# Kernel tuning notes

Hardware: AMD Instinct MI355X
Metric: run time of the kernel (lower is better)

Reference implementation:

```python
import jax, jax.numpy as jnp
import numpy as np

WINDOW_SIZE = 5
CONSISTENCY_WEIGHT = 1.0


def _wsum(x, w):
    # sliding-window sum along axis 1 via exclusive cumsum differences
    s = jnp.cumsum(x, axis=1)
    s = jnp.pad(s, ((0, 0), (1, 0)))
    return s[:, w:] - s[:, :-w]  # [B, L-w+1]


def setup_inputs() -> dict:
    key = jax.random.key(0)
    k1, k2, k3 = jax.random.split(key, 3)
    B, L, C = 512, 16384, 2
    return {
        "predictions": jax.random.normal(k1, (B, L, C), dtype=jnp.float32),
        "targets": jax.random.randint(k2, (B, L), 0, 2, dtype=jnp.int32),
        "mask": jax.random.randint(k3, (B, L), 0, 2, dtype=jnp.int32),
    }


def reference(predictions, targets, mask):
    w = WINDOW_SIZE
    probs = jax.nn.softmax(predictions, axis=-1)[..., 1]  # [B, L]
    t = targets.astype(jnp.float32)
    m = mask.astype(jnp.float32)

    msum = _wsum(m, w)                       # [B, W]
    denom = jnp.maximum(msum, 1.0)           # clamp(min=1.0)
    spm = _wsum(probs * m, w)
    stm = _wsum(t * m, w)
    sp2m = _wsum(probs * probs * m, w)
    st2m = _wsum(t * t * m, w)

    pmean = spm / denom
    tmean = stm / denom
    # masked biased variance: sum((x - mean)^2 * m) / clamp(msum, 1)
    pvar = (sp2m - 2.0 * pmean * spm + pmean * pmean * msum) / denom
    tvar = (st2m - 2.0 * tmean * stm + tmean * tmean * msum) / denom

    mse = jnp.mean((pvar - tvar) ** 2, axis=0)          # per-window MSE over batch, [W]
    valid = (jnp.sum(msum, axis=0) > 0).astype(jnp.float32)  # skip windows with zero mask
    cnt = jnp.maximum(jnp.sum(valid), 1.0)
    loss = jnp.sum(mse * valid) / cnt * CONSISTENCY_WEIGHT
    return loss
```

## Files before the change

kernel.cpp:

```cpp
#include <hip/hip_runtime.h>
#include <math.h>

#define BATCH 512
#define LEN   16384
#define WIN   5
#define WOUT  (LEN - WIN + 1)
#define TPB   128
#define WPT   4
#define WPB   (TPB * WPT)
#define EPT   (WPT + WIN - 1)

__global__ __launch_bounds__(TPB)
void bcl_partial_kernel(const float* __restrict__ pred,
                        const int*   __restrict__ tgt,
                        const int*   __restrict__ msk,
                        float* __restrict__ part_d2,
                        float* __restrict__ part_ms,
                        int bper) {
    const int j0 = blockIdx.x * WPB + (int)threadIdx.x * WPT;
    if (j0 >= WOUT) return;
    const int b0 = blockIdx.y * bper;

    float accd2[WPT] = {0.f, 0.f, 0.f, 0.f};
    float accms[WPT] = {0.f, 0.f, 0.f, 0.f};

    for (int b = b0; b < b0 + bper; ++b) {
        const size_t base = (size_t)b * LEN + j0;

        const int4 m0 = *(const int4*)(msk + base);
        const int4 m1 = *(const int4*)(msk + base + 4);
        const int4 t0 = *(const int4*)(tgt + base);
        const int4 t1 = *(const int4*)(tgt + base + 4);
        const float4 q0 = *(const float4*)(pred + base * 2);
        const float4 q1 = *(const float4*)(pred + base * 2 + 4);
        const float4 q2 = *(const float4*)(pred + base * 2 + 8);
        const float4 q3 = *(const float4*)(pred + base * 2 + 12);

        float m[EPT], tm[EPT], pm[EPT], p2m[EPT];
        {
            const int mi[EPT] = {m0.x, m0.y, m0.z, m0.w, m1.x, m1.y, m1.z, m1.w};
            const int ti[EPT] = {t0.x, t0.y, t0.z, t0.w, t1.x, t1.y, t1.z, t1.w};
            const float dx[EPT] = {q0.x - q0.y, q0.z - q0.w,
                                   q1.x - q1.y, q1.z - q1.w,
                                   q2.x - q2.y, q2.z - q2.w,
                                   q3.x - q3.y, q3.z - q3.w};
#pragma unroll
            for (int i = 0; i < EPT; ++i) {
                const float p  = 1.0f / (1.0f + __expf(dx[i]));
                const float mf = (float)mi[i];
                m[i]   = mf;
                tm[i]  = (float)(ti[i] & mi[i]);
                pm[i]  = p * mf;
                p2m[i] = p * p * mf;
            }
        }

#pragma unroll
        for (int w = 0; w < WPT; ++w) {
            float msum = 0.f, stm = 0.f, spm = 0.f, sp2m = 0.f;
#pragma unroll
            for (int k = 0; k < WIN; ++k) {
                msum += m[w + k];
                stm  += tm[w + k];
                spm  += pm[w + k];
                sp2m += p2m[w + k];
            }
            const float denom = fmaxf(msum, 1.0f);
            const float inv   = 1.0f / denom;
            const float pmean = spm * inv;
            const float tmean = stm * inv;
            const float pvar  = (sp2m - 2.0f * pmean * spm + pmean * pmean * msum) * inv;
            const float tvar  = (stm  - 2.0f * tmean * stm + tmean * tmean * msum) * inv;
            const float d = pvar - tvar;
            accd2[w] += d * d;
            accms[w] += msum;
        }
    }

    *(float4*)(part_d2 + (size_t)blockIdx.y * WOUT + j0) =
        make_float4(accd2[0], accd2[1], accd2[2], accd2[3]);
    *(float4*)(part_ms + (size_t)blockIdx.y * WOUT + j0) =
        make_float4(accms[0], accms[1], accms[2], accms[3]);
}

__global__ void bcl_window_reduce(const float* __restrict__ part_d2,
                                  const float* __restrict__ part_ms,
                                  double* __restrict__ accum,
                                  unsigned int* __restrict__ ticket,
                                  float* __restrict__ out,
                                  int nchunks) {
    const int j = blockIdx.x * blockDim.x + threadIdx.x;
    double num = 0.0, cnt = 0.0;
    if (j < WOUT) {
        float d2 = 0.f, ms = 0.f;
        for (int c = 0; c < nchunks; ++c) {
            d2 += part_d2[(size_t)c * WOUT + j];
            ms += part_ms[(size_t)c * WOUT + j];
        }
        if (ms > 0.f) {
            num = (double)d2 * (1.0 / (double)BATCH);
            cnt = 1.0;
        }
    }
    for (int off = 32; off > 0; off >>= 1) {
        num += __shfl_down(num, off, 64);
        cnt += __shfl_down(cnt, off, 64);
    }
    __shared__ double s_num[4], s_cnt[4];
    const int lane = threadIdx.x & 63, wave = threadIdx.x >> 6;
    if (lane == 0) { s_num[wave] = num; s_cnt[wave] = cnt; }
    __syncthreads();
    if (threadIdx.x == 0) {
        double n = 0.0, c = 0.0;
        const int nw = (int)(blockDim.x >> 6);
        for (int wv = 0; wv < nw; ++wv) { n += s_num[wv]; c += s_cnt[wv]; }
        atomicAdd(&accum[0], n);
        atomicAdd(&accum[1], c);
        __threadfence();
        const unsigned int t = atomicAdd(ticket, 1u);
        if (t == gridDim.x - 1) {
            out[0] = (float)(accum[0] / fmax(accum[1], 1.0));
        }
    }
}

extern "C" void kernel_launch(void* const* d_in, const int* in_sizes, int n_in,
                              void* d_out, int out_size, void* d_ws, size_t ws_size,
                              hipStream_t stream) {
    const float* pred = (const float*)d_in[0];
    const int*   tgt  = (const int*)d_in[1];
    const int*   msk  = (const int*)d_in[2];
    float* out = (float*)d_out;

    int nchunks = 64;
    while (nchunks > 1) {
        size_t need = (size_t)nchunks * WOUT * 2 * sizeof(float) + 64;
        if (need <= ws_size) break;
        nchunks >>= 1;
    }
    const int bper = BATCH / nchunks;

    float* part_d2 = (float*)d_ws;
    float* part_ms = part_d2 + (size_t)nchunks * WOUT;
    size_t off = ((size_t)nchunks * WOUT * 2 * sizeof(float) + 15) & ~(size_t)15;
    double* accum = (double*)((char*)d_ws + off);
    unsigned int* ticket = (unsigned int*)(accum + 2);

    hipMemsetAsync((void*)accum, 0, 2 * sizeof(double) + sizeof(unsigned int), stream);

    const int WBLKS = (WOUT + WPB - 1) / WPB;
    dim3 g1(WBLKS, nchunks);
    bcl_partial_kernel<<<g1, TPB, 0, stream>>>(pred, tgt, msk, part_d2, part_ms, bper);

    const int RBLKS = (WOUT + 255) / 256;
    bcl_window_reduce<<<RBLKS, 256, 0, stream>>>(part_d2, part_ms, accum, ticket, out, nchunks);
}
```

Measured before the change: 177.5 us.

## Add two-stage chunk reduction, raise batch chunks, use fast reciprocal

New measurement: 166.0 us. -6.5%, faster.

```diff
diff --git a/kernel.cpp b/kernel.cpp
--- a/kernel.cpp
+++ b/kernel.cpp
@@ -5,12 +5,18 @@
 #define LEN   16384
 #define WIN   5
 #define WOUT  (LEN - WIN + 1)
-#define TPB   128
+#define TPB   256
 #define WPT   4
 #define WPB   (TPB * WPT)
 #define EPT   (WPT + WIN - 1)
+#define NCH2  16
 
-__global__ __launch_bounds__(TPB)
+__device__ __forceinline__ float fast_rcp(float x) {
+    float r = __builtin_amdgcn_rcpf(x);
+    return r * fmaf(-x, r, 2.0f);
+}
+
+__global__ __launch_bounds__(TPB, 8)
 void bcl_partial_kernel(const float* __restrict__ pred,
                         const int*   __restrict__ tgt,
                         const int*   __restrict__ msk,
@@ -46,7 +52,7 @@
                                    q3.x - q3.y, q3.z - q3.w};
 #pragma unroll
             for (int i = 0; i < EPT; ++i) {
-                const float p  = 1.0f / (1.0f + __expf(dx[i]));
+                const float p  = fast_rcp(1.0f + __expf(dx[i]));
                 const float mf = (float)mi[i];
                 m[i]   = mf;
                 tm[i]  = (float)(ti[i] & mi[i]);
@@ -66,7 +72,7 @@
                 sp2m += p2m[w + k];
             }
             const float denom = fmaxf(msum, 1.0f);
-            const float inv   = 1.0f / denom;
+            const float inv   = fast_rcp(denom);
             const float pmean = spm * inv;
             const float tmean = stm * inv;
             const float pvar  = (sp2m - 2.0f * pmean * spm + pmean * pmean * msum) * inv;
@@ -83,19 +89,40 @@
         make_float4(accms[0], accms[1], accms[2], accms[3]);
 }
 
-__global__ void bcl_window_reduce(const float* __restrict__ part_d2,
-                                  const float* __restrict__ part_ms,
-                                  double* __restrict__ accum,
-                                  unsigned int* __restrict__ ticket,
-                                  float* __restrict__ out,
-                                  int nchunks) {
+__global__ __launch_bounds__(TPB)
+void bcl_chunk_reduce(const float* __restrict__ part_d2,
+                      const float* __restrict__ part_ms,
+                      float* __restrict__ p2_d2,
+                      float* __restrict__ p2_ms,
+                      int rf) {
+    const int j = blockIdx.x * blockDim.x + threadIdx.x;
+    if (j >= WOUT) return;
+    const int c0 = blockIdx.y * rf;
+    float d2 = 0.f, ms = 0.f;
+#pragma unroll 8
+    for (int c = c0; c < c0 + rf; ++c) {
+        d2 += part_d2[(size_t)c * WOUT + j];
+        ms += part_ms[(size_t)c * WOUT + j];
+    }
+    p2_d2[(size_t)blockIdx.y * WOUT + j] = d2;
+    p2_ms[(size_t)blockIdx.y * WOUT + j] = ms;
+}
+
+__global__ __launch_bounds__(TPB)
+void bcl_window_reduce(const float* __restrict__ p2_d2,
+                       const float* __restrict__ p2_ms,
+                       double* __restrict__ accum,
+                       unsigned int* __restrict__ ticket,
+                       float* __restrict__ out,
+                       int nch2) {
     const int j = blockIdx.x * blockDim.x + threadIdx.x;
     double num = 0.0, cnt = 0.0;
     if (j < WOUT) {
         float d2 = 0.f, ms = 0.f;
-        for (int c = 0; c < nchunks; ++c) {
-            d2 += part_d2[(size_t)c * WOUT + j];
-            ms += part_ms[(size_t)c * WOUT + j];
+#pragma unroll 8
+        for (int c = 0; c < nch2; ++c) {
+            d2 += p2_d2[(size_t)c * WOUT + j];
+            ms += p2_ms[(size_t)c * WOUT + j];
         }
         if (ms > 0.f) {
             num = (double)d2 * (1.0 / (double)BATCH);
@@ -132,17 +159,21 @@
     const int*   msk  = (const int*)d_in[2];
     float* out = (float*)d_out;
 
-    int nchunks = 64;
+    int nchunks = 128;
     while (nchunks > 1) {
-        size_t need = (size_t)nchunks * WOUT * 2 * sizeof(float) + 64;
+        size_t need = (size_t)(nchunks + NCH2) * WOUT * 2 * sizeof(float) + 256;
         if (need <= ws_size) break;
         nchunks >>= 1;
     }
     const int bper = BATCH / nchunks;
+    const int nch2 = (nchunks >= NCH2) ? NCH2 : nchunks;
+    const int rf   = nchunks / nch2;
 
     float* part_d2 = (float*)d_ws;
     float* part_ms = part_d2 + (size_t)nchunks * WOUT;
-    size_t off = ((size_t)nchunks * WOUT * 2 * sizeof(float) + 15) & ~(size_t)15;
+    float* p2_d2   = part_ms + (size_t)nchunks * WOUT;
+    float* p2_ms   = p2_d2   + (size_t)NCH2 * WOUT;
+    size_t off = ((size_t)((char*)(p2_ms + (size_t)NCH2 * WOUT) - (char*)d_ws) + 15) & ~(size_t)15;
     double* accum = (double*)((char*)d_ws + off);
     unsigned int* ticket = (unsigned int*)(accum + 2);
 
@@ -152,6 +183,9 @@
     dim3 g1(WBLKS, nchunks);
     bcl_partial_kernel<<<g1, TPB, 0, stream>>>(pred, tgt, msk, part_d2, part_ms, bper);
 
-    const int RBLKS = (WOUT + 255) / 256;
-    bcl_window_reduce<<<RBLKS, 256, 0, stream>>>(part_d2, part_ms, accum, ticket, out, nchunks);
+    const int RBLKS = (WOUT + TPB - 1) / TPB;
+    dim3 gA(RBLKS, nch2);
+    bcl_chunk_reduce<<<gA, TPB, 0, stream>>>(part_d2, part_ms, p2_d2, p2_ms, rf);
+
+    bcl_window_reduce<<<RBLKS, TPB, 0, stream>>>(p2_d2, p2_ms, accum, ticket, out, nch2);
 }
```
